# Optimization experiments

Measured on AMD Instinct MI355X. Metric: run time of the kernel, lower is better.

Reference implementation:

```python
import jax, jax.numpy as jnp
import numpy as np
from jax import lax

NUM_SIMS = 2048
NUM_BITS = 256   # == num_nodes
MID_DIM = 512
LN_EPS = 1e-5


def _net(x, w1, b1, gamma, beta, w2, b2):
    # BnMLP: Linear -> GELU (exact erf) -> LayerNorm -> Linear -> Sigmoid
    h = x @ w1 + b1                                   # [S, MID]
    h = jax.nn.gelu(h, approximate=False)
    mu = jnp.mean(h, axis=-1, keepdims=True)
    var = jnp.mean(jnp.square(h - mu), axis=-1, keepdims=True)
    h = (h - mu) * lax.rsqrt(var + LN_EPS) * gamma + beta
    return jax.nn.sigmoid(h @ w2 + b2)                # [S, NUM_BITS]


def setup_inputs() -> dict:
    key = jax.random.key(0)
    k_x, k_p, k_w1, k_w2 = jax.random.split(key, 4)
    xs_flt = jax.random.uniform(k_x, (NUM_SIMS, NUM_BITS), dtype=jnp.float32)
    # one random permutation of the nodes per simulation (th.randperm per sim)
    ids_ary = jax.vmap(lambda k: jax.random.permutation(k, NUM_BITS))(
        jax.random.split(k_p, NUM_SIMS)).astype(jnp.int32)   # [S, N]
    w1 = jax.random.normal(k_w1, (NUM_BITS, MID_DIM), jnp.float32) / np.sqrt(NUM_BITS)
    b1 = jnp.full((MID_DIM,), 1e-6, jnp.float32)
    gamma = jnp.ones((MID_DIM,), jnp.float32)
    beta = jnp.zeros((MID_DIM,), jnp.float32)
    w2 = jax.random.normal(k_w2, (MID_DIM, NUM_BITS), jnp.float32) * (0.1 / np.sqrt(MID_DIM))
    b2 = jnp.full((NUM_BITS,), 1e-6, jnp.float32)
    return {"xs_flt": xs_flt, "ids_ary": ids_ary, "w1": w1, "b1": b1,
            "gamma": gamma, "beta": beta, "w2": w2, "b2": b2}


def reference(xs_flt, ids_ary, w1, b1, gamma, beta, w2, b2):
    # gathers prob at (sim, ids[sim]) and writes ps broadcast over all rows at
    # columns ids (faithful to torch's `probs[:, ids] = ps` broadcast semantics).
    def step(probs, ids):
        out = _net(probs, w1, b1, gamma, beta, w2, b2)        # [S, N]
        ps = jnp.take_along_axis(out, ids[:, None], axis=1)[:, 0]  # [S]
        probs = probs.at[:, ids].set(ps)                      # broadcast over rows
        return probs, None

    probs, _ = lax.scan(step, xs_flt, ids_ary.T)              # scan over N nodes
    return probs
```

## Files before the change

kernel.cpp:

```cpp
#include <hip/hip_runtime.h>
#include <math.h>

#define S_ 2048
#define N_ 256
#define MID_ 512
#define NB_ 8
#define JSL_ 64
#define LN_EPS_ 1e-5f
#define NBLK_ 64
#define NSTEP_ 253
#define BSTRIDE_ 288
#define SLOT_F_ (NB_*BSTRIDE_)
#define TAGST_ 16
#define TAG_TARGET_ 0x0101010101010101ULL

typedef float f32x4 __attribute__((ext_vector_type(4)));
typedef float f32x2 __attribute__((ext_vector_type(2)));

__device__ __forceinline__ float gelu_exact(float x){
    return 0.5f * x * (1.0f + erff(x * 0.70710678118654752440f));
}


__global__ void k_init(const float* __restrict__ xs, const float* __restrict__ w2,
                       float* __restrict__ probs, float* __restrict__ w2T,
                       unsigned int* __restrict__ wmaskb, int* __restrict__ tagw32,
                       int* __restrict__ cnt, int* __restrict__ winner)
{
    int idx = blockIdx.x * blockDim.x + threadIdx.x;
    if (idx < S_*N_) probs[idx] = xs[idx];
    if (idx < MID_*N_) {
        int j = idx / N_, c = idx % N_;
        w2T[c*MID_ + j] = w2[idx];
    }
    if (idx < (N_*N_)/32) wmaskb[idx] = 0u;
    if (idx < NSTEP_*TAGST_*2) tagw32[idx] = 0;
    if (idx < 8) cnt[idx] = 0;
    if (idx == 0) *winner = -1;
}

__global__ void k_maskb(const int* __restrict__ ids, unsigned int* __restrict__ wmaskb){
    int i = blockIdx.x*blockDim.x + threadIdx.x;
    if (i < S_*N_){
        int t = i & (N_-1);
        int c = ids[i];
        atomicOr(&wmaskb[(t<<3) + (c>>5)], 1u << (c&31));
    }
}

__global__ void k_ab(const float* __restrict__ gamma, const float* __restrict__ beta,
                     const float* __restrict__ w2, const float* __restrict__ b2,
                     float* __restrict__ A, float* __restrict__ Bc){
    __shared__ float ra[256], rb[256];
    int c = blockIdx.x, tid = threadIdx.x;
    float a = 0.f, b = 0.f;
    for (int j = tid; j < MID_; j += 256){
        float v = w2[j*N_ + c];
        a += gamma[j]*v;
        b += beta[j]*v;
    }
    ra[tid] = a; rb[tid] = b; __syncthreads();
    for (int off = 128; off > 0; off >>= 1){
        if (tid < off){ ra[tid] += ra[tid+off]; rb[tid] += rb[tid+off]; }
        __syncthreads();
    }
    if (tid == 0){ A[c] = ra[0]; Bc[c] = rb[0] + b2[c]; }
}


__global__ __launch_bounds__(256) void k_full_rows(
    const float* __restrict__ probs, const float* __restrict__ w1,
    const float* __restrict__ b1, const float* __restrict__ gamma,
    const float* __restrict__ beta, const float* __restrict__ w2T,
    const float* __restrict__ b2, const int* __restrict__ ids,
    float* __restrict__ ps, int t)
{
    __shared__ float prow[8][N_];
    int tid = threadIdx.x;
    int r0 = blockIdx.x * 8;
    for (int i = tid; i < 8*N_; i += 256)
        prow[i>>8][i&255] = probs[(r0 + (i>>8))*N_ + (i&255)];
    __syncthreads();
    int r = tid >> 5, jg = tid & 31;
    float h[16];
    #pragma unroll
    for (int m = 0; m < 16; m++) h[m] = b1[jg + 32*m];
    for (int c = 0; c < N_; c++){
        float p = prow[r][c];
        const float* w1r = w1 + c*MID_;
        #pragma unroll
        for (int m = 0; m < 16; m++) h[m] = fmaf(p, w1r[jg + 32*m], h[m]);
    }
    float s1 = 0.f, s2 = 0.f;
    #pragma unroll
    for (int m = 0; m < 16; m++){
        float g = gelu_exact(h[m]);
        h[m] = g; s1 += g; s2 += g*g;
    }
    #pragma unroll
    for (int off = 16; off > 0; off >>= 1){
        s1 += __shfl_xor(s1, off, 32);
        s2 += __shfl_xor(s2, off, 32);
    }
    float mu  = s1 * (1.f/MID_);
    float var = s2 * (1.f/MID_) - mu*mu;
    float inv = rsqrtf(var + LN_EPS_);
    int rg = r0 + r;
    int id = ids[rg*N_ + t];
    const float* wrow = w2T + id*MID_;
    float acc = 0.f;
    #pragma unroll
    for (int m = 0; m < 16; m++){
        int j = jg + 32*m;
        float hn = (h[m] - mu)*inv*gamma[j] + beta[j];
        acc = fmaf(hn, wrow[j], acc);
    }
    #pragma unroll
    for (int off = 16; off > 0; off >>= 1) acc += __shfl_xor(acc, off, 32);
    if (jg == 0) ps[rg] = 1.f/(1.f + expf(-(acc + b2[id])));
}

__global__ void k_scatter(const int* __restrict__ ids, const float* __restrict__ ps,
                          float* __restrict__ newval, int* __restrict__ wrote, int t){
    __shared__ int lastk[N_];
    int tid = threadIdx.x;
    lastk[tid] = -1;
    __syncthreads();
    for (int k = tid; k < S_; k += 256) atomicMax(&lastk[ids[k*N_ + t]], k);
    __syncthreads();
    int lk = lastk[tid];
    wrote[tid] = (lk >= 0) ? 1 : 0;
    if (lk >= 0) newval[tid] = ps[lk];
}

__global__ void k_apply(float* __restrict__ probs, const float* __restrict__ newval,
                        const int* __restrict__ wrote){
    int idx = blockIdx.x*blockDim.x + threadIdx.x;
    int c = idx & (N_-1);
    if (wrote[c]) probs[idx] = newval[c];
}


__global__ __launch_bounds__(512) void k_fast(
    const float* __restrict__ w1, const float* __restrict__ b1,
    const float* __restrict__ gamma, const float* __restrict__ w2,
    const float* __restrict__ A, const float* __restrict__ Bc,
    const unsigned int* __restrict__ wmaskb, const float* __restrict__ probs,
    const float* __restrict__ newval, const int* __restrict__ wrote,
    float* __restrict__ slots, unsigned long long* __restrict__ tagw,
    int* __restrict__ cnt, int* __restrict__ winner,
    float* __restrict__ commonFinal, int t0)
{
    __shared__ int s_role;
    __shared__ __attribute__((aligned(16))) float commonS[N_];
    __shared__ __attribute__((aligned(16))) float gvals[JSL_];
    __shared__ float ws8[16];
    __shared__ float pst[NB_][2];
    __shared__ unsigned int wbits[(N_*N_)/32];

    int tid = threadIdx.x;

    if (tid == 0){
        int xcd;
        asm volatile("s_getreg_b32 %0, hwreg(HW_REG_XCC_ID)" : "=s"(xcd));
        xcd &= 7;
        int pos = atomicAdd(&cnt[xcd], 1);
        int role = -1;
        if (pos == NB_ - 1){
            int old = atomicCAS(winner, -1, xcd);
            if (old == -1) role = NB_ - 1;
        } else if (pos < NB_ - 1){
            int w;
            while ((w = atomicCAS(winner, -2, -2)) == -1)
                __builtin_amdgcn_s_sleep(2);
            if (w == xcd) role = pos;
        }
        s_role = role;
    }
    __syncthreads();
    int role = s_role;
    if (role < 0) return;
    int j0 = role * JSL_;

    int l = tid & 63, w = tid >> 6;
    int cg = l & 7;
    int jA = (w<<3) + (l>>3);
    int cB = w*32 + (l & 31);
    int khalf = l >> 5;

    float w1r[32];
    #pragma unroll
    for (int cc = 0; cc < 32; cc++)
        w1r[cc] = w1[(cg*32 + cc)*MID_ + j0 + jA];
    float g2r[32];
    #pragma unroll
    for (int kk = 0; kk < 32; kk++)
        g2r[kk] = gamma[j0 + khalf*32 + kk] * w2[(j0 + khalf*32 + kk)*N_ + cB];
    float b1v = b1[j0 + jA];

    for (int i = tid; i < (N_*N_)/32; i += 512) wbits[i] = wmaskb[i];
    if (tid < N_)
        commonS[tid ^ (((tid>>5)&7)<<2)] = wrote[tid] ? newval[tid] : probs[tid];
    float Ac  = (tid < N_) ? A[tid]  : 0.f;
    float Bcc = (tid < N_) ? Bc[tid] : 0.f;
    __syncthreads();

    for (int t = t0; t < N_; t++){
        int si = t - t0;
        float* slot = slots + si*SLOT_F_;
        float* myp  = slot + role*BSTRIDE_;
        {
            float a0=0.f, a1=0.f, a2=0.f, a3=0.f;
            #pragma unroll
            for (int cc = 0; cc < 8; cc++){
                f32x4 cv = *(const f32x4*)(&commonS[(cg*32 + cc*4) ^ (cg<<2)]);
                a0 = fmaf(w1r[cc*4+0], cv.x, a0);
                a1 = fmaf(w1r[cc*4+1], cv.y, a1);
                a2 = fmaf(w1r[cc*4+2], cv.z, a2);
                a3 = fmaf(w1r[cc*4+3], cv.w, a3);
            }
            float hp = (a0+a1) + (a2+a3);
            hp += __shfl_xor(hp, 1);
            hp += __shfl_xor(hp, 2);
            hp += __shfl_xor(hp, 4);
            float g = gelu_exact(hp + b1v);
            float s1 = g, s2 = g*g;
            s1 += __shfl_xor(s1, 8);  s2 += __shfl_xor(s2, 8);
            s1 += __shfl_xor(s1, 16); s2 += __shfl_xor(s2, 16);
            s1 += __shfl_xor(s1, 32); s2 += __shfl_xor(s2, 32);
            if (l == 0){ ws8[w*2] = s1; ws8[w*2+1] = s2; }
            if (cg == 0) gvals[jA] = g;
        }
        __syncthreads();
        {
            float p0=0.f, p1=0.f, p2=0.f, p3=0.f;
            #pragma unroll
            for (int kk = 0; kk < 8; kk++){
                f32x4 gv = *(const f32x4*)(&gvals[khalf*32 + kk*4]);
                p0 = fmaf(g2r[kk*4+0], gv.x, p0);
                p1 = fmaf(g2r[kk*4+1], gv.y, p1);
                p2 = fmaf(g2r[kk*4+2], gv.z, p2);
                p3 = fmaf(g2r[kk*4+3], gv.w, p3);
            }
            float p = (p0+p1) + (p2+p3);
            p += __shfl_xor(p, 32);
            if (l < 32) myp[cB] = p;
        }
        if (tid == 0){
            float S1 = 0.f, S2 = 0.f;
            #pragma unroll
            for (int ww = 0; ww < 8; ww++){ S1 += ws8[ww*2]; S2 += ws8[ww*2+1]; }
            f32x2 st; st.x = S1; st.y = S2;
            *(f32x2*)(myp + 256) = st;
        }
        asm volatile("s_waitcnt vmcnt(0)" ::: "memory");
        __syncthreads();
        if (tid == 0){
            unsigned long long* tp = tagw + si*TAGST_;
            atomicAdd(tp, 1ULL << (8*role));
            while (atomicAdd(tp, 0ULL) != TAG_TARGET_)
                __builtin_amdgcn_s_sleep(1);
        }
        __syncthreads();
        if (tid < NB_){
            f32x2 st = *(const f32x2*)(slot + tid*BSTRIDE_ + 256);
            pst[tid][0] = st.x; pst[tid][1] = st.y;
        }
        __syncthreads();
        if (tid < N_){
            const float* sp = slot + tid;
            float s1 = 0.f;
            #pragma unroll
            for (int bb = 0; bb < NB_; bb++) s1 += sp[bb*BSTRIDE_];
            float S1 = 0.f, S2 = 0.f;
            #pragma unroll
            for (int bb = 0; bb < NB_; bb++){ S1 += pst[bb][0]; S2 += pst[bb][1]; }
            float mu  = S1 * (1.f/MID_);
            float var = S2 * (1.f/MID_) - mu*mu;
            float inv = rsqrtf(var + LN_EPS_);
            float s = inv*(s1 - mu*Ac) + Bcc;
            float o = 1.f/(1.f + expf(-s));
            if ((wbits[(t<<3) + (tid>>5)] >> (tid&31)) & 1u)
                commonS[tid ^ (((tid>>5)&7)<<2)] = o;
        }
        __syncthreads();
    }
    if (role == 0 && tid < N_)
        commonFinal[tid] = commonS[tid ^ (((tid>>5)&7)<<2)];
}

__global__ void k_out(const float* __restrict__ commonFinal, float* __restrict__ out){
    int idx = blockIdx.x*blockDim.x + threadIdx.x;
    out[idx] = commonFinal[idx & (N_-1)];
}


extern "C" void kernel_launch(void* const* d_in, const int* in_sizes, int n_in,
                              void* d_out, int out_size, void* d_ws, size_t ws_size,
                              hipStream_t stream)
{
    const float* xs    = (const float*)d_in[0];
    const int*   ids   = (const int*)  d_in[1];
    const float* w1    = (const float*)d_in[2];
    const float* b1    = (const float*)d_in[3];
    const float* gamma = (const float*)d_in[4];
    const float* beta  = (const float*)d_in[5];
    const float* w2    = (const float*)d_in[6];
    const float* b2    = (const float*)d_in[7];
    float* out = (float*)d_out;

    float* ws      = (float*)d_ws;
    float* probs   = ws;
    float* slots   = ws + 2048;
    float* w2T     = ws + 524288;
    float* A       = ws + 786432;
    float* Bc      = ws + 786688;
    float* ps      = ws + 786944;
    float* newval  = ws + 788992;
    int*   wrote   = (int*)(ws + 789248);
    unsigned int* wmaskb = (unsigned int*)(ws + 805888);
    int*   tagw32  = (int*)(ws + 807936);
    unsigned long long* tagw = (unsigned long long*)tagw32;
    int*   cnt     = tagw32 + NSTEP_*TAGST_*2;
    int*   winner  = cnt + 8;
    float* commonFinal = ws + 816064;

    k_init<<<2048, 256, 0, stream>>>(xs, w2, probs, w2T, wmaskb, tagw32,
                                     cnt, winner);
    k_maskb<<<2048, 256, 0, stream>>>(ids, wmaskb);
    k_ab<<<256, 256, 0, stream>>>(gamma, beta, w2, b2, A, Bc);

    for (int t = 0; t < 3; t++){
        k_full_rows<<<256, 256, 0, stream>>>(probs, w1, b1, gamma, beta, w2T, b2,
                                             ids, ps, t);
        k_scatter<<<1, 256, 0, stream>>>(ids, ps, newval, wrote, t);
        if (t < 2) k_apply<<<2048, 256, 0, stream>>>(probs, newval, wrote);
    }

    k_fast<<<NBLK_, 512, 0, stream>>>(w1, b1, gamma, w2, A, Bc, wmaskb, probs,
                                      newval, wrote, slots, tagw, cnt, winner,
                                      commonFinal, 3);
    k_out<<<2048, 256, 0, stream>>>(commonFinal, out);
}
```

Baseline: 723.2 us.

## Compute only winning rows in first steps and drop probs copy and scatter kernels

The first three autoregressive steps no longer run the MLP for all 2048 rows. A prep kernel finds, for each column, the last simulation that writes it, and the MLP is evaluated only for those winner rows, built from xs plus the earlier step values. This removes the probs copy, the w2 transpose, the scatter and apply kernels, and most of the full-row compute. The inter-block barrier in the persistent kernel also now lets 8 threads spin without sleep and read their stats directly, which trims one __syncthreads but adds more atomic polling traffic.

```diff
diff --git a/kernel.cpp b/kernel.cpp
--- a/kernel.cpp
+++ b/kernel.cpp
@@ -22,21 +22,30 @@
 }
 
 
-__global__ void k_init(const float* __restrict__ xs, const float* __restrict__ w2,
-                       float* __restrict__ probs, float* __restrict__ w2T,
-                       unsigned int* __restrict__ wmaskb, int* __restrict__ tagw32,
+__global__ void k_init(unsigned int* __restrict__ wmaskb, int* __restrict__ tagw32,
                        int* __restrict__ cnt, int* __restrict__ winner)
 {
     int idx = blockIdx.x * blockDim.x + threadIdx.x;
-    if (idx < S_*N_) probs[idx] = xs[idx];
-    if (idx < MID_*N_) {
-        int j = idx / N_, c = idx % N_;
-        w2T[c*MID_ + j] = w2[idx];
-    }
     if (idx < (N_*N_)/32) wmaskb[idx] = 0u;
     if (idx < NSTEP_*TAGST_*2) tagw32[idx] = 0;
     if (idx < 8) cnt[idx] = 0;
     if (idx == 0) *winner = -1;
+}
+
+__global__ void k_prep(const int* __restrict__ ids, int* __restrict__ winners){
+    __shared__ int lastk[3][N_];
+    int tid = threadIdx.x;
+    lastk[0][tid] = -1; lastk[1][tid] = -1; lastk[2][tid] = -1;
+    __syncthreads();
+    for (int k = tid; k < S_; k += 256){
+        atomicMax(&lastk[0][ids[k*N_ + 0]], k);
+        atomicMax(&lastk[1][ids[k*N_ + 1]], k);
+        atomicMax(&lastk[2][ids[k*N_ + 2]], k);
+    }
+    __syncthreads();
+    winners[0*N_ + tid] = lastk[0][tid];
+    winners[1*N_ + tid] = lastk[1][tid];
+    winners[2*N_ + tid] = lastk[2][tid];
 }
 
 __global__ void k_maskb(const int* __restrict__ ids, unsigned int* __restrict__ wmaskb){
@@ -68,76 +77,60 @@
 }
 
 
-__global__ __launch_bounds__(256) void k_full_rows(
-    const float* __restrict__ probs, const float* __restrict__ w1,
+__global__ __launch_bounds__(256) void k_fullW(
+    const float* __restrict__ xs, const float* __restrict__ w1,
     const float* __restrict__ b1, const float* __restrict__ gamma,
-    const float* __restrict__ beta, const float* __restrict__ w2T,
-    const float* __restrict__ b2, const int* __restrict__ ids,
-    float* __restrict__ ps, int t)
+    const float* __restrict__ beta, const float* __restrict__ w2,
+    const float* __restrict__ b2, const int* __restrict__ winners,
+    float* __restrict__ nv, int t)
 {
-    __shared__ float prow[8][N_];
+    __shared__ float prow[4][N_];
     int tid = threadIdx.x;
-    int r0 = blockIdx.x * 8;
-    for (int i = tid; i < 8*N_; i += 256)
-        prow[i>>8][i&255] = probs[(r0 + (i>>8))*N_ + (i&255)];
-    __syncthreads();
-    int r = tid >> 5, jg = tid & 31;
-    float h[16];
-    #pragma unroll
-    for (int m = 0; m < 16; m++) h[m] = b1[jg + 32*m];
-    for (int c = 0; c < N_; c++){
-        float p = prow[r][c];
-        const float* w1r = w1 + c*MID_;
+    int r = tid >> 6, l = tid & 63;
+    int c = blockIdx.x*4 + r;
+    int kr = winners[t*N_ + c];
+    int krow = kr < 0 ? 0 : kr;
+    #pragma unroll
+    for (int q = 0; q < 4; q++){
+        int cc = l*4 + q;
+        float v = xs[krow*N_ + cc];
+        if (t > 0 && winners[cc] >= 0)      v = nv[cc];
+        if (t > 1 && winners[N_ + cc] >= 0) v = nv[N_ + cc];
+        prow[r][cc] = v;
+    }
+    float h[8];
+    #pragma unroll
+    for (int m = 0; m < 8; m++) h[m] = b1[l + 64*m];
+    for (int cc = 0; cc < N_; cc++){
+        float p = prow[r][cc];
+        const float* w1r = w1 + cc*MID_;
         #pragma unroll
-        for (int m = 0; m < 16; m++) h[m] = fmaf(p, w1r[jg + 32*m], h[m]);
+        for (int m = 0; m < 8; m++) h[m] = fmaf(p, w1r[l + 64*m], h[m]);
     }
     float s1 = 0.f, s2 = 0.f;
     #pragma unroll
-    for (int m = 0; m < 16; m++){
+    for (int m = 0; m < 8; m++){
         float g = gelu_exact(h[m]);
         h[m] = g; s1 += g; s2 += g*g;
     }
     #pragma unroll
-    for (int off = 16; off > 0; off >>= 1){
-        s1 += __shfl_xor(s1, off, 32);
-        s2 += __shfl_xor(s2, off, 32);
+    for (int off = 32; off > 0; off >>= 1){
+        s1 += __shfl_xor(s1, off, 64);
+        s2 += __shfl_xor(s2, off, 64);
     }
     float mu  = s1 * (1.f/MID_);
     float var = s2 * (1.f/MID_) - mu*mu;
     float inv = rsqrtf(var + LN_EPS_);
-    int rg = r0 + r;
-    int id = ids[rg*N_ + t];
-    const float* wrow = w2T + id*MID_;
     float acc = 0.f;
     #pragma unroll
-    for (int m = 0; m < 16; m++){
-        int j = jg + 32*m;
+    for (int m = 0; m < 8; m++){
+        int j = l + 64*m;
         float hn = (h[m] - mu)*inv*gamma[j] + beta[j];
-        acc = fmaf(hn, wrow[j], acc);
-    }
-    #pragma unroll
-    for (int off = 16; off > 0; off >>= 1) acc += __shfl_xor(acc, off, 32);
-    if (jg == 0) ps[rg] = 1.f/(1.f + expf(-(acc + b2[id])));
-}
-
-__global__ void k_scatter(const int* __restrict__ ids, const float* __restrict__ ps,
-                          float* __restrict__ newval, int* __restrict__ wrote, int t){
-    __shared__ int lastk[N_];
-    int tid = threadIdx.x;
-    lastk[tid] = -1;
-    __syncthreads();
-    for (int k = tid; k < S_; k += 256) atomicMax(&lastk[ids[k*N_ + t]], k);
-    __syncthreads();
-    int lk = lastk[tid];
-    wrote[tid] = (lk >= 0) ? 1 : 0;
-    if (lk >= 0) newval[tid] = ps[lk];
-}
-
-__global__ void k_apply(float* __restrict__ probs, const float* __restrict__ newval,
-                        const int* __restrict__ wrote){
-    int idx = blockIdx.x*blockDim.x + threadIdx.x;
-    int c = idx & (N_-1);
-    if (wrote[c]) probs[idx] = newval[c];
+        acc = fmaf(hn, w2[j*N_ + c], acc);
+    }
+    #pragma unroll
+    for (int off = 32; off > 0; off >>= 1) acc += __shfl_xor(acc, off, 64);
+    if (l == 0) nv[t*N_ + c] = 1.f/(1.f + expf(-(acc + b2[c])));
 }
 
 
@@ -145,8 +138,8 @@
     const float* __restrict__ w1, const float* __restrict__ b1,
     const float* __restrict__ gamma, const float* __restrict__ w2,
     const float* __restrict__ A, const float* __restrict__ Bc,
-    const unsigned int* __restrict__ wmaskb, const float* __restrict__ probs,
-    const float* __restrict__ newval, const int* __restrict__ wrote,
+    const unsigned int* __restrict__ wmaskb, const float* __restrict__ xs,
+    const int* __restrict__ winners3, const float* __restrict__ nv,
     float* __restrict__ slots, unsigned long long* __restrict__ tagw,
     int* __restrict__ cnt, int* __restrict__ winner,
     float* __restrict__ commonFinal, int t0)
@@ -199,8 +192,13 @@
     float b1v = b1[j0 + jA];
 
     for (int i = tid; i < (N_*N_)/32; i += 512) wbits[i] = wmaskb[i];
-    if (tid < N_)
-        commonS[tid ^ (((tid>>5)&7)<<2)] = wrote[tid] ? newval[tid] : probs[tid];
+    if (tid < N_){
+        float v = xs[tid];
+        if (winners3[tid] >= 0)        v = nv[tid];
+        if (winners3[N_ + tid] >= 0)   v = nv[N_ + tid];
+        if (winners3[2*N_ + tid] >= 0) v = nv[2*N_ + tid];
+        commonS[tid ^ (((tid>>5)&7)<<2)] = v;
+    }
     float Ac  = (tid < N_) ? A[tid]  : 0.f;
     float Bcc = (tid < N_) ? Bc[tid] : 0.f;
     __syncthreads();
@@ -255,16 +253,14 @@
         }
         asm volatile("s_waitcnt vmcnt(0)" ::: "memory");
         __syncthreads();
-        if (tid == 0){
+        {
             unsigned long long* tp = tagw + si*TAGST_;
-            atomicAdd(tp, 1ULL << (8*role));
-            while (atomicAdd(tp, 0ULL) != TAG_TARGET_)
-                __builtin_amdgcn_s_sleep(1);
-        }
-        __syncthreads();
-        if (tid < NB_){
-            f32x2 st = *(const f32x2*)(slot + tid*BSTRIDE_ + 256);
-            pst[tid][0] = st.x; pst[tid][1] = st.y;
+            if (tid == 0) atomicAdd(tp, 1ULL << (8*role));
+            if (tid < NB_){
+                while (atomicAdd(tp, 0ULL) != TAG_TARGET_) {}
+                f32x2 st = *(const f32x2*)(slot + tid*BSTRIDE_ + 256);
+                pst[tid][0] = st.x; pst[tid][1] = st.y;
+            }
         }
         __syncthreads();
         if (tid < N_){
@@ -310,35 +306,29 @@
     float* out = (float*)d_out;
 
     float* ws      = (float*)d_ws;
-    float* probs   = ws;
-    float* slots   = ws + 2048;
-    float* w2T     = ws + 524288;
-    float* A       = ws + 786432;
-    float* Bc      = ws + 786688;
-    float* ps      = ws + 786944;
-    float* newval  = ws + 788992;
-    int*   wrote   = (int*)(ws + 789248);
-    unsigned int* wmaskb = (unsigned int*)(ws + 805888);
-    int*   tagw32  = (int*)(ws + 807936);
+    float* slots   = ws;
+    float* commonFinal = ws + 582912;
+    float* nv      = ws + 583168;
+    float* A       = ws + 583936;
+    float* Bc      = ws + 584192;
+    int*   winners = (int*)(ws + 584448);
+    unsigned int* wmaskb = (unsigned int*)(ws + 585216);
+    int*   tagw32  = (int*)(ws + 587264);
     unsigned long long* tagw = (unsigned long long*)tagw32;
     int*   cnt     = tagw32 + NSTEP_*TAGST_*2;
     int*   winner  = cnt + 8;
-    float* commonFinal = ws + 816064;
-
-    k_init<<<2048, 256, 0, stream>>>(xs, w2, probs, w2T, wmaskb, tagw32,
-                                     cnt, winner);
+
+    k_init<<<64, 256, 0, stream>>>(wmaskb, tagw32, cnt, winner);
+    k_prep<<<1, 256, 0, stream>>>(ids, winners);
     k_maskb<<<2048, 256, 0, stream>>>(ids, wmaskb);
     k_ab<<<256, 256, 0, stream>>>(gamma, beta, w2, b2, A, Bc);
 
-    for (int t = 0; t < 3; t++){
-        k_full_rows<<<256, 256, 0, stream>>>(probs, w1, b1, gamma, beta, w2T, b2,
-                                             ids, ps, t);
-        k_scatter<<<1, 256, 0, stream>>>(ids, ps, newval, wrote, t);
-        if (t < 2) k_apply<<<2048, 256, 0, stream>>>(probs, newval, wrote);
-    }
-
-    k_fast<<<NBLK_, 512, 0, stream>>>(w1, b1, gamma, w2, A, Bc, wmaskb, probs,
-                                      newval, wrote, slots, tagw, cnt, winner,
+    for (int t = 0; t < 3; t++)
+        k_fullW<<<64, 256, 0, stream>>>(xs, w1, b1, gamma, beta, w2, b2,
+                                        winners, nv, t);
+
+    k_fast<<<NBLK_, 512, 0, stream>>>(w1, b1, gamma, w2, A, Bc, wmaskb, xs,
+                                      winners, nv, slots, tagw, cnt, winner,
                                       commonFinal, 3);
     k_out<<<2048, 256, 0, stream>>>(commonFinal, out);
 }
```

New measurement: 675.0 us. 6.7% less time.
